# Kernel optimization log

Hardware: AMD Instinct MI355X
Metric: run time of the kernel (lower is better)

The kernel has to match this reference:

```python
import jax, jax.numpy as jnp
import numpy as np

N_NODES = 50000
N_EDGES = 600000
N_ELEMENTS = 100
N_RBF = 50
D = 128
CUTOFF = 5.0


def setup_inputs() -> dict:
    key = jax.random.key(0)
    ks = jax.random.split(key, 10)
    node_type = jax.random.randint(ks[0], (N_NODES,), 0, N_ELEMENTS)
    x_nodes = jax.random.normal(ks[1], (N_NODES, D), dtype=jnp.float32)
    src = jax.random.randint(ks[2], (N_EDGES,), 0, N_NODES)
    dst = jax.random.randint(ks[3], (N_EDGES,), 0, N_NODES)
    rbf_edges = jax.random.normal(ks[4], (N_EDGES, N_RBF), dtype=jnp.float32)
    dist = jax.random.uniform(ks[5], (N_EDGES,), dtype=jnp.float32) * (CUTOFF * 1.2)
    emb = jax.random.normal(ks[6], (N_ELEMENTS, D), dtype=jnp.float32) * 0.1
    W_e = jax.random.normal(ks[7], (D, N_RBF), dtype=jnp.float32) * (1.0 / np.sqrt(N_RBF))
    b_e = jnp.zeros((D,), dtype=jnp.float32)
    W_c = jax.random.normal(ks[8], (D, 2 * D), dtype=jnp.float32) * (1.0 / np.sqrt(2 * D))
    b_c = jnp.zeros((D,), dtype=jnp.float32)
    return {"node_type": node_type, "x_nodes": x_nodes, "src": src, "dst": dst,
            "rbf_edges": rbf_edges, "dist": dist, "emb": emb,
            "W_e": W_e, "b_e": b_e, "W_c": W_c, "b_c": b_c}


def cosine_cutoff(dist, cutoff):
    # 0.5*(cos(pi*d/cutoff)+1), zeroed beyond cutoff
    w = 0.5 * (jnp.cos(dist * (jnp.pi / cutoff)) + 1.0)
    return w * (dist < cutoff).astype(dist.dtype)


def reference(node_type, x_nodes, src, dst, rbf_edges, dist, emb, W_e, b_e, W_c, b_c):
    # node embedding from atom type: [N, D]
    x_neighbors = emb[node_type]
    # edge projection weighted by cutoff: [E, D]
    x_edges = (rbf_edges @ W_e.T + b_e) * cosine_cutoff(dist, CUTOFF)[:, None]
    # gather source node embedding, multiply by edge embedding, scatter-sum to dst
    msg = x_neighbors[src] * x_edges  # [E, D]
    x_integrated = jax.ops.segment_sum(msg, dst, num_segments=N_NODES)  # [N, D]
    # concat + combine linear: [N, D]
    x_combine = jnp.concatenate([x_nodes, x_integrated], axis=-1)
    return x_combine @ W_c.T + b_c
```

## Files before the change

kernel.cpp:

```cpp
#include <hip/hip_runtime.h>
#include <hip/hip_bf16.h>

constexpr int NN   = 50000;
constexpr int NE   = 600000;
constexpr int NRBF = 50;
constexpr int DIM  = 128;
constexpr float CUT = 5.0f;
constexpr float PI_F = 3.14159265358979323846f;

constexpr int CAP = 32;

constexpr size_t OFF_DEG   = 0;
constexpr size_t OFF_OVFC  = (size_t)NN * 4;
constexpr size_t OFF_EBUF  = 200960;
constexpr size_t OFF_OVF   = OFF_EBUF + (size_t)NN * CAP * 16;
constexpr size_t OFF_WAUG  = OFF_OVF  + (size_t)NE * 4;
constexpr size_t OFF_EPERM = OFF_WAUG + 128 * 64 * 2;
constexpr size_t OFF_XI    = OFF_EPERM + 100 * 128 * 2;


typedef __attribute__((ext_vector_type(4))) float f32x4;
typedef __attribute__((ext_vector_type(8))) short short8;

__device__ __forceinline__ float bf2f(unsigned short u) {
    return __uint_as_float(((unsigned int)u) << 16);
}
__device__ __forceinline__ unsigned short f2bf(float f) {
    return __bfloat16_as_ushort(__float2bfloat16(f));
}

__global__ __launch_bounds__(256)
void bucket_prep(const int* __restrict__ dst, const float* __restrict__ dist,
                 const int* __restrict__ src, const int* __restrict__ node_type,
                 int* __restrict__ deg, int4* __restrict__ ebuf,
                 int* __restrict__ ovf, int* __restrict__ ovf_cnt,
                 const float* __restrict__ W_e, const float* __restrict__ b_e,
                 const float* __restrict__ emb,
                 unsigned short* __restrict__ W_aug, unsigned short* __restrict__ emb_perm)
{
    const int e = blockIdx.x * 256 + threadIdx.x;

    if (e < NE) {
        const float dd = dist[e];
        if (dd < CUT) {
            const float w = 0.5f * (__cosf(dd * (PI_F / CUT)) + 1.0f);
            const int n = dst[e];
            const int pos = atomicAdd(&deg[n], 1);
            if (pos < CAP) {
                ebuf[(size_t)n * CAP + pos] =
                    make_int4(e, __float_as_int(w), node_type[src[e]], 0);
            } else {
                ovf[atomicAdd(ovf_cnt, 1)] = e;
            }
        }
    }

    if (e < 128 * 64) {
        const int d = e >> 6, k = e & 63;
        float v = 0.0f;
        if (k < NRBF)       v = W_e[d * NRBF + k];
        else if (k == NRBF) v = b_e[d];
        W_aug[e] = f2bf(v);
    } else if (e < 128 * 64 + 100 * 128) {
        const int i = e - 128 * 64;
        const int tau = i >> 7, p = i & 127;
        const int d = 16 * (p & 7) + (p >> 3);
        emb_perm[i] = f2bf(emb[tau * DIM + d]);
    }
}

struct NodeLoad {
    float2 r0, r1, r2, r3, q0, q1, q2, q3;
    float  ccl;
    int    degn;
    int    mb;
};

__device__ __forceinline__ void issue_node(const int4* __restrict__ eb_s,
                                           const int* __restrict__ deg_s,
                                           const float* __restrict__ rbf,
                                           int nl, int c, int g, NodeLoad& L)
{
    const int dn = deg_s[nl];
    L.degn = dn < CAP ? dn : CAP;
    L.mb   = nl * 32;
    int ea = 0; L.ccl = 0.0f;
    if (c < L.degn) {
        const int4 eb = eb_s[L.mb + c];
        ea    = eb.x;
        L.ccl = __int_as_float(eb.y);
    }
    const float2* rp2 = (const float2*)(rbf + (size_t)ea * NRBF);
    L.r0 = rp2[4 * g];     L.r1 = rp2[4 * g + 1];
    L.r2 = rp2[4 * g + 2]; L.r3 = rp2[4 * g + 3];
    L.q0 = make_float2(0.f, 0.f); L.q1 = L.q0; L.q2 = L.q0; L.q3 = L.q0;
    if (g < 2) {
        L.q0 = rp2[16 + 4 * g]; L.q1 = rp2[17 + 4 * g];
        L.q2 = rp2[18 + 4 * g]; L.q3 = rp2[19 + 4 * g];
    } else if (g == 2) {
        L.q0 = rp2[24];
    }
}

__device__ __forceinline__ void round_compute(
    float ccl, float2 r0, float2 r1, float2 r2, float2 r3,
    float2 q0, float2 q1, float2 q2, float2 q3,
    int j0, int degn, int mb, int c, int g,
    const unsigned short* __restrict__ wlds, const int4* __restrict__ eb_s,
    const unsigned short* __restrict__ emb_perm, float v[8])
{
    short8 a0, a1;
    a0[0] = (short)f2bf(ccl * r0.x); a0[1] = (short)f2bf(ccl * r0.y);
    a0[2] = (short)f2bf(ccl * r1.x); a0[3] = (short)f2bf(ccl * r1.y);
    a0[4] = (short)f2bf(ccl * r2.x); a0[5] = (short)f2bf(ccl * r2.y);
    a0[6] = (short)f2bf(ccl * r3.x); a0[7] = (short)f2bf(ccl * r3.y);
    a1[0] = (short)f2bf(ccl * q0.x); a1[1] = (short)f2bf(ccl * q0.y);
    a1[2] = (short)f2bf(ccl * q1.x); a1[3] = (short)f2bf(ccl * q1.y);
    a1[4] = (short)f2bf(ccl * q2.x); a1[5] = (short)f2bf(ccl * q2.y);
    a1[6] = (short)f2bf(ccl * q3.x); a1[7] = (short)f2bf(ccl * q3.y);
    if (g == 2) {
        a1[2] = (short)f2bf(ccl);
        a1[3] = 0; a1[4] = 0; a1[5] = 0; a1[6] = 0; a1[7] = 0;
    }

    f32x4 acc[8] = {};
    #pragma unroll
    for (int nt = 0; nt < 8; ++nt) {
        const short8 bf0 = *(const short8*)((const char*)wlds + (nt * 16 + c) * 144 + g * 16);
        acc[nt] = __builtin_amdgcn_mfma_f32_16x16x32_bf16(a0, bf0, acc[nt], 0, 0, 0);
    }
    #pragma unroll
    for (int nt = 0; nt < 8; ++nt) {
        const short8 bf1 = *(const short8*)((const char*)wlds + (nt * 16 + c) * 144 + (4 + g) * 16);
        acc[nt] = __builtin_amdgcn_mfma_f32_16x16x32_bf16(a1, bf1, acc[nt], 0, 0, 0);
    }

    #pragma unroll
    for (int r = 0; r < 4; ++r) {
        const int jr = j0 + 4 * g + r;
        if (jr < degn) {
            const int rw = eb_s[mb + jr].z;
            const int4 em = *(const int4*)(emb_perm + rw * DIM + 8 * c);
            const unsigned int* ep = (const unsigned int*)&em;
            #pragma unroll
            for (int q = 0; q < 4; ++q) {
                const float m0 = bf2f((unsigned short)(ep[q] & 0xffff));
                const float m1 = bf2f((unsigned short)(ep[q] >> 16));
                v[2 * q]     += bf2f(f2bf(acc[2 * q][r]     * m0));
                v[2 * q + 1] += bf2f(f2bf(acc[2 * q + 1][r] * m1));
            }
        }
    }
}

__device__ __forceinline__ void compute_node(
    const NodeLoad& L, int c, int g,
    const unsigned short* __restrict__ wlds, const int4* __restrict__ eb_s,
    const unsigned short* __restrict__ emb_perm, const float* __restrict__ rbf,
    float v[8])
{
    round_compute(L.ccl, L.r0, L.r1, L.r2, L.r3, L.q0, L.q1, L.q2, L.q3,
                  0, L.degn, L.mb, c, g, wlds, eb_s, emb_perm, v);
    if (L.degn > 16) {
        int ea = 0; float ccl = 0.0f;
        const int slot = 16 + c;
        if (slot < L.degn) {
            const int4 eb = eb_s[L.mb + slot];
            ea  = eb.x;
            ccl = __int_as_float(eb.y);
        }
        const float2* rp2 = (const float2*)(rbf + (size_t)ea * NRBF);
        const float2 r0 = rp2[4 * g],     r1 = rp2[4 * g + 1];
        const float2 r2 = rp2[4 * g + 2], r3 = rp2[4 * g + 3];
        float2 q0 = make_float2(0.f, 0.f), q1 = q0, q2 = q0, q3 = q0;
        if (g < 2) {
            q0 = rp2[16 + 4 * g]; q1 = rp2[17 + 4 * g];
            q2 = rp2[18 + 4 * g]; q3 = rp2[19 + 4 * g];
        } else if (g == 2) {
            q0 = rp2[24];
        }
        round_compute(ccl, r0, r1, r2, r3, q0, q1, q2, q3,
                      16, L.degn, L.mb, c, g, wlds, eb_s, emb_perm, v);
    }
}

__device__ __forceinline__ void finish_node(
    float v[8], int n, int c, int g, int ocnt,
    const int* __restrict__ ovf, const int* __restrict__ dst,
    const float* __restrict__ dist, const int* __restrict__ src,
    const int* __restrict__ node_type, const float* __restrict__ rbf,
    const unsigned short* __restrict__ W_aug_g,
    const unsigned short* __restrict__ emb_perm, unsigned short* __restrict__ xi)
{
    for (int j = 0; j < ocnt; ++j) {
        const int e = ovf[j];
        if (dst[e] != n) continue;
        const float dd  = dist[e];
        const float ccl = 0.5f * (__cosf(dd * (PI_F / CUT)) + 1.0f);
        if (g == 0) {
            const int tau = node_type[src[e]];
            const float* rp = rbf + (size_t)e * NRBF;
            const float ccb16 = bf2f(f2bf(ccl));
            #pragma unroll
            for (int q = 0; q < 8; ++q) {
                const int d = 16 * q + c;
                float s = bf2f(W_aug_g[d * 64 + NRBF]) * ccb16;
                for (int k = 0; k < NRBF; ++k)
                    s += bf2f(W_aug_g[d * 64 + k]) * bf2f(f2bf(ccl * rp[k]));
                v[q] += bf2f(f2bf(s * bf2f(emb_perm[tau * DIM + 8 * c + q])));
            }
        }
    }

    #pragma unroll
    for (int q = 0; q < 8; ++q) {
        v[q] += __shfl_xor(v[q], 16);
        v[q] += __shfl_xor(v[q], 32);
    }

    float s0 = v[0], s1 = v[1];
    if (g == 1)      { s0 = v[2]; s1 = v[3]; }
    else if (g == 2) { s0 = v[4]; s1 = v[5]; }
    else if (g == 3) { s0 = v[6]; s1 = v[7]; }
    if (n < NN) {
        xi[(size_t)n * DIM + 32 * g + c]      = f2bf(s0);
        xi[(size_t)n * DIM + 32 * g + 16 + c] = f2bf(s1);
    }
}

__global__ __launch_bounds__(256)
void gather_fused(const float* __restrict__ rbf,
                  const int* __restrict__ deg, const int4* __restrict__ ebuf,
                  const unsigned short* __restrict__ W_aug,
                  const unsigned short* __restrict__ emb_perm,
                  const int* __restrict__ ovf, const int* __restrict__ ovf_cnt,
                  const int* __restrict__ dst, const float* __restrict__ dist,
                  const int* __restrict__ src, const int* __restrict__ node_type,
                  unsigned short* __restrict__ xi)
{
    __shared__ __align__(16) unsigned short wlds[128 * 72];
    __shared__ int4 eb_s[8 * 32];
    __shared__ int  deg_s[8];

    const int t = threadIdx.x, l = t & 63;
    const int wv = t >> 6;
    const int c = l & 15, g = l >> 4;
    const int n0 = blockIdx.x * 8;

    {
        eb_s[t] = ebuf[(size_t)n0 * CAP + t];
        if (t < 8) deg_s[t] = (n0 + t < NN) ? deg[n0 + t] : 0;
        #pragma unroll
        for (int i = 0; i < 4; ++i) {
            const int ch = i * 256 + t;
            const int row = ch >> 3, f = ch & 7;
            *(int4*)((char*)wlds + row * 144 + f * 16) = ((const int4*)W_aug)[ch];
        }
    }
    __syncthreads();
    const int ocnt = ovf_cnt[0];

    const int nbase = wv * 2;

    NodeLoad L0, L1;
    issue_node(eb_s, deg_s, rbf, nbase + 0, c, g, L0);
    issue_node(eb_s, deg_s, rbf, nbase + 1, c, g, L1);

    {
        float v[8] = {};
        compute_node(L0, c, g, wlds, eb_s, emb_perm, rbf, v);
        finish_node(v, n0 + nbase + 0, c, g, ocnt, ovf, dst, dist, src,
                    node_type, rbf, W_aug, emb_perm, xi);
    }
    {
        float v[8] = {};
        compute_node(L1, c, g, wlds, eb_s, emb_perm, rbf, v);
        finish_node(v, n0 + nbase + 1, c, g, ocnt, ovf, dst, dist, src,
                    node_type, rbf, W_aug, emb_perm, xi);
    }
}

__global__ __launch_bounds__(256)
void combine_mfma(const float* __restrict__ x_nodes, const __hip_bfloat16* __restrict__ xi,
                  const float* __restrict__ W_c, const float* __restrict__ b_c,
                  float* __restrict__ out)
{
    __shared__ unsigned short As[64][72];
    __shared__ unsigned short Bs[128][72];

    const int t  = threadIdx.x;
    const int wv = t >> 6;
    const int l  = t & 63;
    const int n0 = blockIdx.x * 64;

    f32x4 acc[8] = {};

    for (int kc = 0; kc < 4; ++kc) {
        const int kb = kc * 64;
        if (kc) __syncthreads();
        {
            const int r  = t >> 2;
            const int c0 = (t & 3) * 16;
            const int n  = n0 + r;
            if (kc < 2) {
                float4 v[4];
                if (n < NN) {
                    const float4* p = (const float4*)(x_nodes + (size_t)n * DIM + kb + c0);
                    v[0] = p[0]; v[1] = p[1]; v[2] = p[2]; v[3] = p[3];
                } else {
                    v[0] = v[1] = v[2] = v[3] = make_float4(0.f, 0.f, 0.f, 0.f);
                }
                unsigned short* dp = &As[r][c0];
                #pragma unroll
                for (int q = 0; q < 4; ++q) {
                    *(ushort2*)&dp[q * 4]     = make_ushort2(f2bf(v[q].x), f2bf(v[q].y));
                    *(ushort2*)&dp[q * 4 + 2] = make_ushort2(f2bf(v[q].z), f2bf(v[q].w));
                }
            } else {
                int4 v0 = make_int4(0, 0, 0, 0), v1 = make_int4(0, 0, 0, 0);
                if (n < NN) {
                    const int4* p = (const int4*)(xi + (size_t)n * DIM + (kb - DIM) + c0);
                    v0 = p[0];
                    v1 = p[1];
                }
                *(int4*)&As[r][c0]     = v0;
                *(int4*)&As[r][c0 + 8] = v1;
            }
        }
        {
            const int dch = t >> 1;
            const int c0  = (t & 1) * 32;
            const float4* p = (const float4*)(W_c + (size_t)dch * (2 * DIM) + kb + c0);
            unsigned short* dp = &Bs[dch][c0];
            #pragma unroll
            for (int q = 0; q < 8; ++q) {
                const float4 v = p[q];
                *(ushort2*)&dp[q * 4]     = make_ushort2(f2bf(v.x), f2bf(v.y));
                *(ushort2*)&dp[q * 4 + 2] = make_ushort2(f2bf(v.z), f2bf(v.w));
            }
        }
        __syncthreads();
        #pragma unroll
        for (int s = 0; s < 2; ++s) {
            const int ko = s * 32 + (l >> 4) * 8;
            const short8 af = *(const short8*)&As[wv * 16 + (l & 15)][ko];
            #pragma unroll
            for (int nt = 0; nt < 8; ++nt) {
                const short8 bf = *(const short8*)&Bs[nt * 16 + (l & 15)][ko];
                acc[nt] = __builtin_amdgcn_mfma_f32_16x16x32_bf16(af, bf, acc[nt], 0, 0, 0);
            }
        }
    }

    const int col = l & 15;
    const int rq  = (l >> 4) * 4;
    #pragma unroll
    for (int nt = 0; nt < 8; ++nt) {
        const int dim = nt * 16 + col;
        const float bc = b_c[dim];
        #pragma unroll
        for (int r = 0; r < 4; ++r) {
            const int node = n0 + wv * 16 + rq + r;
            if (node < NN)
                out[(size_t)node * DIM + dim] = acc[nt][r] + bc;
        }
    }
}

extern "C" void kernel_launch(void* const* d_in, const int* in_sizes, int n_in,
                              void* d_out, int out_size, void* d_ws, size_t ws_size,
                              hipStream_t stream)
{
    const int*   node_type = (const int*)  d_in[0];
    const float* x_nodes   = (const float*)d_in[1];
    const int*   src       = (const int*)  d_in[2];
    const int*   dst       = (const int*)  d_in[3];
    const float* rbf       = (const float*)d_in[4];
    const float* dist      = (const float*)d_in[5];
    const float* emb       = (const float*)d_in[6];
    const float* W_e       = (const float*)d_in[7];
    const float* b_e       = (const float*)d_in[8];
    const float* W_c       = (const float*)d_in[9];
    const float* b_c       = (const float*)d_in[10];
    float* out = (float*)d_out;

    char* ws = (char*)d_ws;
    int*            deg      = (int*)(ws + OFF_DEG);
    int*            ovf_cnt  = (int*)(ws + OFF_OVFC);
    int4*           ebuf     = (int4*)(ws + OFF_EBUF);
    int*            ovf      = (int*)(ws + OFF_OVF);
    unsigned short* W_aug    = (unsigned short*)(ws + OFF_WAUG);
    unsigned short* emb_perm = (unsigned short*)(ws + OFF_EPERM);
    unsigned short* xi       = (unsigned short*)(ws + OFF_XI);

    hipMemsetAsync(deg, 0, (NN + 1) * sizeof(int), stream);

    bucket_prep<<<(NE + 255) / 256, 256, 0, stream>>>(
        dst, dist, src, node_type, deg, ebuf, ovf, ovf_cnt,
        W_e, b_e, emb, W_aug, emb_perm);

    gather_fused<<<(NN + 7) / 8, 256, 0, stream>>>(
        rbf, deg, ebuf, W_aug, emb_perm,
        ovf, ovf_cnt, dst, dist, src, node_type, xi);

    combine_mfma<<<(NN + 63) / 64, 256, 0, stream>>>(
        x_nodes, (const __hip_bfloat16*)xi, W_c, b_c, out);
}
```

Baseline: 355.6 us.

## Fuse combine GEMM into gather kernel and pre-convert W_c to bf16

The node-combine matmul now runs inside the gather kernel. x_nodes and the aggregated messages are staged in LDS, which removes the bf16 xi round trip through global memory and one kernel launch. W_c is converted to bf16 once in the prep kernel and read directly from global memory by every block. The trade-offs are MFMA tiles that are half padded (only 8 nodes per block), repeated W_c reads from cache, and extra LDS use.

```diff
diff --git a/kernel.cpp b/kernel.cpp
--- a/kernel.cpp
+++ b/kernel.cpp
@@ -16,7 +16,7 @@
 constexpr size_t OFF_OVF   = OFF_EBUF + (size_t)NN * CAP * 16;
 constexpr size_t OFF_WAUG  = OFF_OVF  + (size_t)NE * 4;
 constexpr size_t OFF_EPERM = OFF_WAUG + 128 * 64 * 2;
-constexpr size_t OFF_XI    = OFF_EPERM + 100 * 128 * 2;
+constexpr size_t OFF_WCB   = OFF_EPERM + 100 * 128 * 2;
 
 
 typedef __attribute__((ext_vector_type(4))) float f32x4;
@@ -35,8 +35,9 @@
                  int* __restrict__ deg, int4* __restrict__ ebuf,
                  int* __restrict__ ovf, int* __restrict__ ovf_cnt,
                  const float* __restrict__ W_e, const float* __restrict__ b_e,
-                 const float* __restrict__ emb,
-                 unsigned short* __restrict__ W_aug, unsigned short* __restrict__ emb_perm)
+                 const float* __restrict__ emb, const float* __restrict__ W_c,
+                 unsigned short* __restrict__ W_aug, unsigned short* __restrict__ emb_perm,
+                 unsigned short* __restrict__ W_cb)
 {
     const int e = blockIdx.x * 256 + threadIdx.x;
 
@@ -66,6 +67,9 @@
         const int tau = i >> 7, p = i & 127;
         const int d = 16 * (p & 7) + (p >> 3);
         emb_perm[i] = f2bf(emb[tau * DIM + d]);
+    } else if (e < 128 * 64 + 100 * 128 + 128 * 256) {
+        const int i = e - (128 * 64 + 100 * 128);
+        W_cb[i] = f2bf(W_c[i]);
     }
 }
 
@@ -139,7 +143,7 @@
     for (int r = 0; r < 4; ++r) {
         const int jr = j0 + 4 * g + r;
         if (jr < degn) {
-            const int rw = eb_s[mb + jr].z;
+            const int rw = ((const int*)&eb_s[mb + jr])[2];
             const int4 em = *(const int4*)(emb_perm + rw * DIM + 8 * c);
             const unsigned int* ep = (const unsigned int*)&em;
             #pragma unroll
@@ -184,13 +188,14 @@
     }
 }
 
-__device__ __forceinline__ void finish_node(
-    float v[8], int n, int c, int g, int ocnt,
+__device__ __forceinline__ void finish_node_lds(
+    float v[8], int n, int nl, int c, int g, int ocnt,
     const int* __restrict__ ovf, const int* __restrict__ dst,
     const float* __restrict__ dist, const int* __restrict__ src,
     const int* __restrict__ node_type, const float* __restrict__ rbf,
     const unsigned short* __restrict__ W_aug_g,
-    const unsigned short* __restrict__ emb_perm, unsigned short* __restrict__ xi)
+    const unsigned short* __restrict__ emb_perm,
+    unsigned short* __restrict__ cat_s )
 {
     for (int j = 0; j < ocnt; ++j) {
         const int e = ovf[j];
@@ -222,23 +227,24 @@
     if (g == 1)      { s0 = v[2]; s1 = v[3]; }
     else if (g == 2) { s0 = v[4]; s1 = v[5]; }
     else if (g == 3) { s0 = v[6]; s1 = v[7]; }
-    if (n < NN) {
-        xi[(size_t)n * DIM + 32 * g + c]      = f2bf(s0);
-        xi[(size_t)n * DIM + 32 * g + 16 + c] = f2bf(s1);
-    }
+    cat_s[nl * 264 + 128 + 32 * g + c]      = f2bf(s0);
+    cat_s[nl * 264 + 128 + 32 * g + 16 + c] = f2bf(s1);
 }
 
 __global__ __launch_bounds__(256)
-void gather_fused(const float* __restrict__ rbf,
-                  const int* __restrict__ deg, const int4* __restrict__ ebuf,
-                  const unsigned short* __restrict__ W_aug,
-                  const unsigned short* __restrict__ emb_perm,
-                  const int* __restrict__ ovf, const int* __restrict__ ovf_cnt,
-                  const int* __restrict__ dst, const float* __restrict__ dist,
-                  const int* __restrict__ src, const int* __restrict__ node_type,
-                  unsigned short* __restrict__ xi)
+void gather_combine(const float* __restrict__ rbf,
+                    const int* __restrict__ deg, const int4* __restrict__ ebuf,
+                    const unsigned short* __restrict__ W_aug,
+                    const unsigned short* __restrict__ emb_perm,
+                    const unsigned short* __restrict__ W_cb,
+                    const int* __restrict__ ovf, const int* __restrict__ ovf_cnt,
+                    const int* __restrict__ dst, const float* __restrict__ dist,
+                    const int* __restrict__ src, const int* __restrict__ node_type,
+                    const float* __restrict__ x_nodes, const float* __restrict__ b_c,
+                    float* __restrict__ out)
 {
     __shared__ __align__(16) unsigned short wlds[128 * 72];
+    __shared__ __align__(16) unsigned short cat_s[16 * 264];
     __shared__ int4 eb_s[8 * 32];
     __shared__ int  deg_s[8];
 
@@ -249,120 +255,53 @@
 
     {
         eb_s[t] = ebuf[(size_t)n0 * CAP + t];
-        if (t < 8) deg_s[t] = (n0 + t < NN) ? deg[n0 + t] : 0;
+        if (t < 8) deg_s[t] = deg[n0 + t];
         #pragma unroll
         for (int i = 0; i < 4; ++i) {
             const int ch = i * 256 + t;
             const int row = ch >> 3, f = ch & 7;
             *(int4*)((char*)wlds + row * 144 + f * 16) = ((const int4*)W_aug)[ch];
         }
+        const int nl = t >> 5, k0 = (t & 31) * 4;
+        const float4 xv = *(const float4*)(x_nodes + (size_t)(n0 + nl) * DIM + k0);
+        *(ushort2*)&cat_s[nl * 264 + k0]     = make_ushort2(f2bf(xv.x), f2bf(xv.y));
+        *(ushort2*)&cat_s[nl * 264 + k0 + 2] = make_ushort2(f2bf(xv.z), f2bf(xv.w));
     }
     __syncthreads();
     const int ocnt = ovf_cnt[0];
 
     const int nbase = wv * 2;
-
-    NodeLoad L0, L1;
-    issue_node(eb_s, deg_s, rbf, nbase + 0, c, g, L0);
-    issue_node(eb_s, deg_s, rbf, nbase + 1, c, g, L1);
-
-    {
+    #pragma unroll
+    for (int ni = 0; ni < 2; ++ni) {
+        const int nl = nbase + ni;
+        NodeLoad L;
+        issue_node(eb_s, deg_s, rbf, nl, c, g, L);
         float v[8] = {};
-        compute_node(L0, c, g, wlds, eb_s, emb_perm, rbf, v);
-        finish_node(v, n0 + nbase + 0, c, g, ocnt, ovf, dst, dist, src,
-                    node_type, rbf, W_aug, emb_perm, xi);
-    }
-    {
-        float v[8] = {};
-        compute_node(L1, c, g, wlds, eb_s, emb_perm, rbf, v);
-        finish_node(v, n0 + nbase + 1, c, g, ocnt, ovf, dst, dist, src,
-                    node_type, rbf, W_aug, emb_perm, xi);
-    }
-}
-
-__global__ __launch_bounds__(256)
-void combine_mfma(const float* __restrict__ x_nodes, const __hip_bfloat16* __restrict__ xi,
-                  const float* __restrict__ W_c, const float* __restrict__ b_c,
-                  float* __restrict__ out)
-{
-    __shared__ unsigned short As[64][72];
-    __shared__ unsigned short Bs[128][72];
-
-    const int t  = threadIdx.x;
-    const int wv = t >> 6;
-    const int l  = t & 63;
-    const int n0 = blockIdx.x * 64;
-
-    f32x4 acc[8] = {};
-
-    for (int kc = 0; kc < 4; ++kc) {
-        const int kb = kc * 64;
-        if (kc) __syncthreads();
-        {
-            const int r  = t >> 2;
-            const int c0 = (t & 3) * 16;
-            const int n  = n0 + r;
-            if (kc < 2) {
-                float4 v[4];
-                if (n < NN) {
-                    const float4* p = (const float4*)(x_nodes + (size_t)n * DIM + kb + c0);
-                    v[0] = p[0]; v[1] = p[1]; v[2] = p[2]; v[3] = p[3];
-                } else {
-                    v[0] = v[1] = v[2] = v[3] = make_float4(0.f, 0.f, 0.f, 0.f);
-                }
-                unsigned short* dp = &As[r][c0];
-                #pragma unroll
-                for (int q = 0; q < 4; ++q) {
-                    *(ushort2*)&dp[q * 4]     = make_ushort2(f2bf(v[q].x), f2bf(v[q].y));
-                    *(ushort2*)&dp[q * 4 + 2] = make_ushort2(f2bf(v[q].z), f2bf(v[q].w));
-                }
-            } else {
-                int4 v0 = make_int4(0, 0, 0, 0), v1 = make_int4(0, 0, 0, 0);
-                if (n < NN) {
-                    const int4* p = (const int4*)(xi + (size_t)n * DIM + (kb - DIM) + c0);
-                    v0 = p[0];
-                    v1 = p[1];
-                }
-                *(int4*)&As[r][c0]     = v0;
-                *(int4*)&As[r][c0 + 8] = v1;
-            }
-        }
-        {
-            const int dch = t >> 1;
-            const int c0  = (t & 1) * 32;
-            const float4* p = (const float4*)(W_c + (size_t)dch * (2 * DIM) + kb + c0);
-            unsigned short* dp = &Bs[dch][c0];
-            #pragma unroll
-            for (int q = 0; q < 8; ++q) {
-                const float4 v = p[q];
-                *(ushort2*)&dp[q * 4]     = make_ushort2(f2bf(v.x), f2bf(v.y));
-                *(ushort2*)&dp[q * 4 + 2] = make_ushort2(f2bf(v.z), f2bf(v.w));
-            }
-        }
-        __syncthreads();
-        #pragma unroll
-        for (int s = 0; s < 2; ++s) {
-            const int ko = s * 32 + (l >> 4) * 8;
-            const short8 af = *(const short8*)&As[wv * 16 + (l & 15)][ko];
-            #pragma unroll
-            for (int nt = 0; nt < 8; ++nt) {
-                const short8 bf = *(const short8*)&Bs[nt * 16 + (l & 15)][ko];
-                acc[nt] = __builtin_amdgcn_mfma_f32_16x16x32_bf16(af, bf, acc[nt], 0, 0, 0);
-            }
-        }
-    }
-
-    const int col = l & 15;
-    const int rq  = (l >> 4) * 4;
-    #pragma unroll
-    for (int nt = 0; nt < 8; ++nt) {
-        const int dim = nt * 16 + col;
-        const float bc = b_c[dim];
-        #pragma unroll
-        for (int r = 0; r < 4; ++r) {
-            const int node = n0 + wv * 16 + rq + r;
-            if (node < NN)
-                out[(size_t)node * DIM + dim] = acc[nt][r] + bc;
+        compute_node(L, c, g, wlds, eb_s, emb_perm, rbf, v);
+        finish_node_lds(v, n0 + nl, nl, c, g, ocnt, ovf, dst, dist, src,
+                        node_type, rbf, W_aug, emb_perm, cat_s);
+    }
+    __syncthreads();
+
+    f32x4 acc0 = {}, acc1 = {};
+    const int t0 = wv * 2, t1 = wv * 2 + 1;
+    #pragma unroll
+    for (int kc = 0; kc < 8; ++kc) {
+        const int ko = kc * 32 + g * 8;
+        const short8 af = *(const short8*)&cat_s[c * 264 + ko];
+        const short8 b0 = *(const short8*)(W_cb + (size_t)(t0 * 16 + c) * 256 + ko);
+        const short8 b1 = *(const short8*)(W_cb + (size_t)(t1 * 16 + c) * 256 + ko);
+        acc0 = __builtin_amdgcn_mfma_f32_16x16x32_bf16(af, b0, acc0, 0, 0, 0);
+        acc1 = __builtin_amdgcn_mfma_f32_16x16x32_bf16(af, b1, acc1, 0, 0, 0);
+    }
+    const float bc0 = b_c[t0 * 16 + c];
+    const float bc1 = b_c[t1 * 16 + c];
+    #pragma unroll
+    for (int r = 0; r < 4; ++r) {
+        const int node = 4 * g + r;
+        if (node < 8) {
+            out[(size_t)(n0 + node) * DIM + t0 * 16 + c] = acc0[r] + bc0;
+            out[(size_t)(n0 + node) * DIM + t1 * 16 + c] = acc1[r] + bc1;
         }
     }
 }
@@ -391,18 +330,15 @@
     int*            ovf      = (int*)(ws + OFF_OVF);
     unsigned short* W_aug    = (unsigned short*)(ws + OFF_WAUG);
     unsigned short* emb_perm = (unsigned short*)(ws + OFF_EPERM);
-    unsigned short* xi       = (unsigned short*)(ws + OFF_XI);
+    unsigned short* W_cb     = (unsigned short*)(ws + OFF_WCB);
 
     hipMemsetAsync(deg, 0, (NN + 1) * sizeof(int), stream);
 
     bucket_prep<<<(NE + 255) / 256, 256, 0, stream>>>(
         dst, dist, src, node_type, deg, ebuf, ovf, ovf_cnt,
-        W_e, b_e, emb, W_aug, emb_perm);
-
-    gather_fused<<<(NN + 7) / 8, 256, 0, stream>>>(
-        rbf, deg, ebuf, W_aug, emb_perm,
-        ovf, ovf_cnt, dst, dist, src, node_type, xi);
-
-    combine_mfma<<<(NN + 63) / 64, 256, 0, stream>>>(
-        x_nodes, (const __hip_bfloat16*)xi, W_c, b_c, out);
-}
+        W_e, b_e, emb, W_c, W_aug, emb_perm, W_cb);
+
+    gather_combine<<<NN / 8, 256, 0, stream>>>(
+        rbf, deg, ebuf, W_aug, emb_perm, W_cb,
+        ovf, ovf_cnt, dst, dist, src, node_type, x_nodes, b_c, out);
+}
```

After: 360.9 us. About the same (+1.5%).
